# Performance work log

Hardware: AMD Instinct MI355X
Metric: run time of the kernel (lower is better)

The kernel has to match this reference:

```python
import jax, jax.numpy as jnp
import numpy as np

DIM = 768; NH = 8; G = 14; N = G * G + 1; B = 64; PD = DIM // 16; HID = 4 * DIM
SCOPES = (1, 4, 7)


def _build_adj(fs, scope):
    # windowed adjacency on an fs x fs grid, padded with an always-on ACM (class) token
    idx = np.arange(fs)
    ii, jj = np.meshgrid(idx, idx, indexing='ij')
    ri, rj = ii.ravel(), jj.ravel()
    a = ((np.abs(ri[:, None] - ri[None, :]) <= scope) & (np.abs(rj[:, None] - rj[None, :]) <= scope)).astype(np.float32)
    out = np.ones((fs * fs + 1, fs * fs + 1), np.float32)
    out[1:, 1:] = a
    return out


def _prior_adj():
    # loop=0 -> loop1=loop2=0, repeat = NH//4; heads get [adj1,adj1,adj2,adj2,adj3,adj3,ones,ones]
    rep = NH // 4
    mats = [_build_adj(G, s) for s in SCOPES] + [np.ones((N, N), np.float32)]
    return np.stack([m for m in mats for _ in range(rep)], 0)


def _rel_idx():
    coords = np.stack(np.meshgrid(np.arange(G), np.arange(G), indexing='ij')).reshape(2, -1)
    rel = (coords[:, :, None] - coords[:, None, :]).transpose(1, 2, 0).copy()
    rel[..., 0] += G - 1
    rel[..., 1] += G - 1
    rel[..., 0] *= 2 * G - 1
    idx = rel.sum(-1)
    out = np.full((N, N), (2 * G - 1) ** 2 + 1, np.int32)
    out[1:, 1:] = idx
    return out


def _biases():
    r = np.arange(-G, G + 1)  # arange(1-(G+1), G+1)
    g = np.stack(np.meshgrid(r, r, indexing='ij')).reshape(2, -1).T
    return g.astype(np.float32)  # ((2G+1)^2, 2)


def setup_inputs():
    key = jax.random.key(0)
    ks = iter(jax.random.split(key, 32))
    rn = lambda *s: jax.random.normal(next(ks), s, jnp.float32) * 0.02
    return dict(
        x=jax.random.normal(next(ks), (B, N, DIM), jnp.float32),
        norm1_w=jnp.ones(DIM), norm1_b=jnp.zeros(DIM),
        qkv_w=rn(3 * DIM, DIM),
        scale=10.0 * jnp.ones((NH, 1, 1)),
        pp_w=rn(PD, 2), pp_b=jnp.zeros(PD),
        ln1_w=jnp.ones(PD), ln1_b=jnp.zeros(PD), fcp1_w=rn(PD, PD), fcp1_b=jnp.zeros(PD),
        ln2_w=jnp.ones(PD), ln2_b=jnp.zeros(PD), fcp2_w=rn(PD, PD), fcp2_b=jnp.zeros(PD),
        ln3_w=jnp.ones(PD), ln3_b=jnp.zeros(PD), fcp3_w=rn(NH, PD), fcp3_b=jnp.zeros(NH),
        pre_w=rn(NH, NH) + jnp.eye(NH), post_w=rn(NH, NH) + jnp.eye(NH),
        proj_w=rn(DIM, DIM), proj_b=jnp.zeros(DIM),
        norm2_w=jnp.ones(DIM), norm2_b=jnp.zeros(DIM),
        m1_w=rn(HID, DIM), m1_b=jnp.zeros(HID),
        m2_w=rn(DIM, HID), m2_b=jnp.zeros(DIM),
        prior_adj=jnp.asarray(_prior_adj()),
        biases=jnp.asarray(_biases()),
        rel_idx=jnp.asarray(_rel_idx()),
    )


def _ln(x, w, b, eps=1e-5):
    m = x.mean(-1, keepdims=True)
    v = ((x - m) ** 2).mean(-1, keepdims=True)
    return (x - m) / jnp.sqrt(v + eps) * w + b


def _l2n(x, eps=1e-12):
    return x / jnp.maximum(jnp.linalg.norm(x, axis=-1, keepdims=True), eps)


def reference(x, norm1_w, norm1_b, qkv_w, scale, pp_w, pp_b, ln1_w, ln1_b, fcp1_w, fcp1_b, ln2_w, ln2_b, fcp2_w, fcp2_b, ln3_w, ln3_b, fcp3_w, fcp3_b, pre_w, post_w, proj_w, proj_b, norm2_w, norm2_b, m1_w, m1_b, m2_w, m2_b, prior_adj, biases, rel_idx):
    Bq, Nq, C = x.shape
    d = C // NH
    h = _ln(x, norm1_w, norm1_b)
    qkv = (h @ qkv_w.T).reshape(Bq, Nq, 3, NH, d).transpose(2, 0, 3, 1, 4)
    q, k, v = qkv[0], qkv[1], qkv[2]  # each (B, NH, N, d)
    attn = jnp.einsum('bhnd,bhmd->bhnm', _l2n(q), _l2n(k)) * jnp.minimum(scale, 100.0)[None]
    p = biases @ pp_w.T + pp_b
    p = jax.nn.relu(_ln(p, ln1_w, ln1_b)) @ fcp1_w.T + fcp1_b
    p = jax.nn.relu(_ln(p, ln2_w, ln2_b)) @ fcp2_w.T + fcp2_b
    p = jax.nn.relu(_ln(p, ln3_w, ln3_b)) @ fcp3_w.T + fcp3_b  # (841, NH)
    rpb = p[rel_idx]  # (N, N, NH)
    attn = attn + rpb.transpose(2, 0, 1)[None]
    attn = jnp.einsum('oh,bhnm->bonm', pre_w, attn)  # 1x1 conv over heads (pre-softmax)
    attn = jnp.where(prior_adj[None] > 0, attn, -1e9)
    attn = jax.nn.softmax(attn, axis=-1)
    attn = jnp.einsum('oh,bhnm->bonm', post_w, attn)  # 1x1 conv over heads (post-softmax)
    out = jnp.einsum('bhnm,bhmd->bhnd', attn, v).transpose(0, 2, 1, 3).reshape(Bq, Nq, C)
    x = x + (out @ proj_w.T + proj_b)
    h2 = _ln(x, norm2_w, norm2_b)
    h2 = jax.nn.gelu(h2 @ m1_w.T + m1_b, approximate=False) @ m2_w.T + m2_b
    return x + h2
```

## Files before the change

kernel.cpp:

```cpp
#include <hip/hip_runtime.h>
#include <hip/hip_bf16.h>
#include <math.h>

typedef __hip_bfloat16 bf16;
typedef __attribute__((ext_vector_type(8))) short bf16x8;
typedef __attribute__((ext_vector_type(4))) float f32x4;

__device__ __forceinline__ float b2f(bf16 x){ return __bfloat162float(x); }
__device__ __forceinline__ bf16  f2b(float x){ return __float2bfloat16(x); }

__device__ __forceinline__ void gld16(const bf16* g, bf16* l){
    __builtin_amdgcn_global_load_lds(
        (const __attribute__((address_space(1))) unsigned int*)g,
        (__attribute__((address_space(3))) unsigned int*)l, 16, 0, 0);
}

#define NTOK 197
#define NBATCH 64
#define NHEAD 8
#define DHEAD 96
#define DIMC 768
#define NROWS (NBATCH * NTOK)
#define VTS 224
#define SMS 228
#define MHALF 6304

#define OFF_P   0ull
#define OFF_W   32768ull
#define SZ_QKVW 3538944ull
#define SZ_PRJW 1179648ull
#define SZ_M1W  4718592ull
#define SZ_M2W  4718592ull
#define OFF_H   14188544ull
#define SZ_H    19365888ull
#define OFF_Q   33554432ull
#define OFF_K   52920320ull
#define OFF_V   72286208ull

__global__ __launch_bounds__(256) void w_cvt_all(
    const float* __restrict__ s0, const float* __restrict__ s1,
    const float* __restrict__ s2, const float* __restrict__ s3, bf16* __restrict__ d)
{
    int i = blockIdx.x*256 + threadIdx.x;
    const float* s; int off;
    if (i < 442368){ s=s0; off=i; }
    else if (i < 589824){ s=s1; off=i-442368; }
    else if (i < 1179648){ s=s2; off=i-589824; }
    else { s=s3; off=i-1179648; }
    float4 v = ((const float4*)s)[off];
    bf16 t[4] = {f2b(v.x), f2b(v.y), f2b(v.z), f2b(v.w)};
    ((ushort4*)d)[i] = *(ushort4*)t;
}

__global__ __launch_bounds__(64) void pos_mlp(
    const float* __restrict__ biases, const float* __restrict__ pp_w, const float* __restrict__ pp_b,
    const float* __restrict__ ln1w, const float* __restrict__ ln1b,
    const float* __restrict__ f1w,  const float* __restrict__ f1b,
    const float* __restrict__ ln2w, const float* __restrict__ ln2b,
    const float* __restrict__ f2w,  const float* __restrict__ f2b,
    const float* __restrict__ ln3w, const float* __restrict__ ln3b,
    const float* __restrict__ f3w,  const float* __restrict__ f3b,
    float* __restrict__ pout)
{
    const int row = blockIdx.x, j = threadIdx.x;
    __shared__ float va[48], vb[48];
    float b0 = biases[row*2], b1 = biases[row*2+1];
    if (j < 48) va[j] = b0*pp_w[j*2] + b1*pp_w[j*2+1] + pp_b[j];
    __syncthreads();
    {   float s=0.f, s2=0.f;
        for (int i=0;i<48;i++){ float t=va[i]; s+=t; s2+=t*t; }
        float mean=s*(1.f/48.f), var=s2*(1.f/48.f)-mean*mean, inv=rsqrtf(var+1e-5f);
        float r=0.f;
        if (j < 48){
            r = f1b[j];
            for (int i=0;i<48;i++){
                float t = fmaxf((va[i]-mean)*inv*ln1w[i] + ln1b[i], 0.f);
                r += t * f1w[j*48+i];
            }
        }
        __syncthreads();
        if (j < 48) vb[j] = r;
    }
    __syncthreads();
    {   float s=0.f, s2=0.f;
        for (int i=0;i<48;i++){ float t=vb[i]; s+=t; s2+=t*t; }
        float mean=s*(1.f/48.f), var=s2*(1.f/48.f)-mean*mean, inv=rsqrtf(var+1e-5f);
        float r=0.f;
        if (j < 48){
            r = f2b[j];
            for (int i=0;i<48;i++){
                float t = fmaxf((vb[i]-mean)*inv*ln2w[i] + ln2b[i], 0.f);
                r += t * f2w[j*48+i];
            }
        }
        __syncthreads();
        if (j < 48) va[j] = r;
    }
    __syncthreads();
    {   float s=0.f, s2=0.f;
        for (int i=0;i<48;i++){ float t=va[i]; s+=t; s2+=t*t; }
        float mean=s*(1.f/48.f), var=s2*(1.f/48.f)-mean*mean, inv=rsqrtf(var+1e-5f);
        if (j < 8){
            float r = f3b[j];
            for (int i=0;i<48;i++){
                float t = fmaxf((va[i]-mean)*inv*ln3w[i] + ln3b[i], 0.f);
                r += t * f3w[j*48+i];
            }
            pout[row*8+j] = r;
        }
    }
}

__device__ __forceinline__ float ldf(const bf16& x){ return __bfloat162float(x); }
__device__ __forceinline__ float ldf(const float& x){ return x; }

template<typename TIN>
__global__ __launch_bounds__(256) void ln768(
    const TIN* __restrict__ x, const float* __restrict__ w, const float* __restrict__ b,
    bf16* __restrict__ out)
{
    const int row = blockIdx.x, tid = threadIdx.x;
    const int wv = tid >> 6, ln = tid & 63;
    __shared__ float rs[4], rs2[4];
    const TIN* xr = x + (size_t)row * DIMC;
    float v0 = ldf(xr[tid]), v1 = ldf(xr[tid+256]), v2 = ldf(xr[tid+512]);
    float s = v0+v1+v2, s2 = v0*v0+v1*v1+v2*v2;
    #pragma unroll
    for (int off=32; off; off>>=1){ s += __shfl_xor(s,off,64); s2 += __shfl_xor(s2,off,64); }
    if (ln == 0){ rs[wv]=s; rs2[wv]=s2; }
    __syncthreads();
    s = rs[0]+rs[1]+rs[2]+rs[3]; s2 = rs2[0]+rs2[1]+rs2[2]+rs2[3];
    float mean = s*(1.f/768.f), var = s2*(1.f/768.f) - mean*mean;
    float inv = rsqrtf(var + 1e-5f);
    size_t base = (size_t)row * DIMC;
    out[base+tid]     = f2b((v0-mean)*inv*w[tid]     + b[tid]);
    out[base+tid+256] = f2b((v1-mean)*inv*w[tid+256] + b[tid+256]);
    out[base+tid+512] = f2b((v2-mean)*inv*w[tid+512] + b[tid+512]);
}

__global__ __launch_bounds__(256) void l2norm_qk(bf16* __restrict__ q, bf16* __restrict__ k)
{
    const int wv = threadIdx.x >> 6, ln = threadIdx.x & 63;
    const size_t NR = (size_t)NBATCH*NHEAD*NTOK;
    size_t row = (size_t)blockIdx.x * 4 + wv;
    bf16* ptr = (row < NR) ? (q + row*DHEAD) : (k + (row-NR)*DHEAD);
    float x0 = b2f(ptr[ln]);
    float x1 = (ln < 32) ? b2f(ptr[64+ln]) : 0.f;
    float ss = x0*x0 + x1*x1;
    #pragma unroll
    for (int off=32; off; off>>=1) ss += __shfl_xor(ss,off,64);
    float inv = 1.f / fmaxf(sqrtf(ss), 1e-12f);
    ptr[ln] = f2b(x0*inv);
    if (ln < 32) ptr[64+ln] = f2b(x1*inv);
}

__global__ __launch_bounds__(256) void attn_mfma(
    const bf16* __restrict__ q, const bf16* __restrict__ k, const bf16* __restrict__ vt,
    const float* __restrict__ p, const float* __restrict__ scale,
    const float* __restrict__ pre_w, const float* __restrict__ post_w,
    bf16* __restrict__ ao)
{
    const int id = blockIdx.x;
    const int r8 = id & 7, t8 = id >> 3;
    const int bx = t8 % 25, b = r8 + 8*(t8/25);
    const int n0 = bx*8;
    const int tid = threadIdx.x, wv = tid>>6, ln = tid&63;
    const int fr = ln&15, fq = ln>>4;
    __shared__ float S[NHEAD*8*SMS];
    __shared__ float s_pre[64], s_post[64], s_sc[8];
    bf16* Sb = (bf16*)S;
    if (tid < 64){ s_pre[tid]=pre_w[tid]; s_post[tid]=post_w[tid]; }
    if (tid < 8)  s_sc[tid] = fminf(scale[tid], 100.f);

    #pragma unroll
    for (int hh=0; hh<2; hh++){
        const int h = wv + hh*4;
        int qr = n0 + fr; if (qr > 196) qr = 196;
        const bf16* qrow = q + ((size_t)(b*NHEAD+h)*NTOK + qr)*DHEAD + fq*8;
        bf16x8 a0 = *(const bf16x8*)(qrow);
        bf16x8 a1 = *(const bf16x8*)(qrow+32);
        bf16x8 a2 = *(const bf16x8*)(qrow+64);
        const bf16* kb0 = k + (size_t)(b*NHEAD+h)*NTOK*DHEAD + fq*8;
        const bf16* kr = kb0 + (size_t)fr*DHEAD;
        bf16x8 kv0 = *(const bf16x8*)(kr);
        bf16x8 kv1 = *(const bf16x8*)(kr+32);
        bf16x8 kv2 = *(const bf16x8*)(kr+64);
        for (int mt=0; mt<13; mt++){
            bf16x8 c0=kv0, c1=kv1, c2=kv2;
            if (mt < 12){
                int nr = (mt+1)*16+fr; if (nr>196) nr=196;
                const bf16* kn = kb0 + (size_t)nr*DHEAD;
                kv0 = *(const bf16x8*)(kn);
                kv1 = *(const bf16x8*)(kn+32);
                kv2 = *(const bf16x8*)(kn+64);
            }
            f32x4 acc = {};
            acc = __builtin_amdgcn_mfma_f32_16x16x32_bf16(a0, c0, acc,0,0,0);
            acc = __builtin_amdgcn_mfma_f32_16x16x32_bf16(a1, c1, acc,0,0,0);
            acc = __builtin_amdgcn_mfma_f32_16x16x32_bf16(a2, c2, acc,0,0,0);
            if (fq < 2){
                #pragma unroll
                for (int i=0;i<4;i++)
                    S[(h*8 + fq*4+i)*SMS + mt*16+fr] = acc[i];
            }
        }
    }
    __syncthreads();

    const int sco[8] = {1,1,4,4,7,7,1000,1000};
    for (int c=tid; c<8*224; c+=256){
        int nq = c/224, m = c - nq*224;
        if (m >= 197){
            #pragma unroll
            for (int o=0;o<8;o++) S[(o*8+nq)*SMS+m] = -1e9f;
            continue;
        }
        int n = n0+nq; if (n > 196) n = 196;
        bool always = (n==0) || (m==0);
        int ri=0, ci=0, rj=0, cj=0;
        if (!always){
            ri=(n-1)/14; ci=(n-1)-ri*14;
            rj=(m-1)/14; cj=(m-1)-rj*14;
        }
        int dr = ri-rj; if (dr<0) dr=-dr;
        int dc = ci-cj; if (dc<0) dc=-dc;
        int idx = always ? 730 : (ri-rj+13)*27 + (ci-cj+13);
        const float* pv = p + idx*8;
        float sh[8];
        #pragma unroll
        for (int h=0;h<8;h++) sh[h] = S[(h*8+nq)*SMS+m]*s_sc[h] + pv[h];
        float ov[8];
        #pragma unroll
        for (int o=0;o<8;o++){
            float v=0.f;
            #pragma unroll
            for (int hh2=0;hh2<8;hh2++) v += s_pre[o*8+hh2]*sh[hh2];
            bool on = always || (dr<=sco[o] && dc<=sco[o]);
            ov[o] = on ? v : -1e9f;
        }
        #pragma unroll
        for (int o=0;o<8;o++) S[(o*8+nq)*SMS+m] = ov[o];
    }
    __syncthreads();

    for (int r = wv*16; r < wv*16+16; r++){
        float* row = &S[r*SMS];
        float mx = -3e38f;
        for (int m=ln; m<224; m+=64) mx = fmaxf(mx, row[m]);
        #pragma unroll
        for (int off=32; off; off>>=1) mx = fmaxf(mx, __shfl_xor(mx,off,64));
        float sum = 0.f;
        for (int m=ln; m<224; m+=64){ float e=__expf(row[m]-mx); row[m]=e; sum+=e; }
        #pragma unroll
        for (int off=32; off; off>>=1) sum += __shfl_xor(sum,off,64);
        float inv = 1.f/sum;
        for (int m=ln; m<224; m+=64) row[m] *= inv;
    }
    __syncthreads();

    float ov[7][8];
    #pragma unroll
    for (int kk=0; kk<7; kk++){
        int c = tid + kk*256;
        if (c < 8*197){
            int nq = c/197, m = c - nq*197;
            float ph[8];
            #pragma unroll
            for (int o=0;o<8;o++) ph[o] = S[(o*8+nq)*SMS+m];
            #pragma unroll
            for (int o2=0;o2<8;o2++){
                float v=0.f;
                #pragma unroll
                for (int o=0;o<8;o++) v += s_post[o2*8+o]*ph[o];
                ov[kk][o2]=v;
            }
        }
    }
    __syncthreads();
    #pragma unroll
    for (int kk=0; kk<7; kk++){
        int c = tid + kk*256;
        if (c < 8*197){
            int nq = c/197, m = c - nq*197;
            #pragma unroll
            for (int o=0;o<8;o++) Sb[(o*8+nq)*456 + m] = f2b(ov[kk][o]);
        }
    }
    for (int i=tid; i<64*27; i+=256){
        int r = i/27, mm = 197 + (i - (i/27)*27);
        Sb[r*456 + mm] = f2b(0.f);
    }
    __syncthreads();

    const int frA = fr & 7;
    #pragma unroll
    for (int hh=0; hh<2; hh++){
        const int h = wv + hh*4;
        const bf16* vbase = vt + (size_t)(b*NHEAD+h)*DHEAD*VTS;
        for (int dt=0; dt<6; dt++){
            f32x4 acc = {};
            #pragma unroll
            for (int ks=0; ks<7; ks++){
                const bf16* ap = Sb + (h*8+frA)*456 + ks*32 + fq*8;
                const bf16* bp = vbase + (size_t)(dt*16+fr)*VTS + ks*32 + fq*8;
                acc = __builtin_amdgcn_mfma_f32_16x16x32_bf16(*(const bf16x8*)ap, *(const bf16x8*)bp, acc,0,0,0);
            }
            #pragma unroll
            for (int i=0;i<4;i++){
                int nq = fq*4+i, n = n0+nq;
                if (nq < 8 && n < NTOK)
                    ao[((size_t)b*NTOK+n)*DIMC + h*DHEAD + dt*16+fr] = f2b(acc[i]);
            }
        }
    }
}

enum { EPI_QKV=0, EPI_X1=1, EPI_GELU=2, EPI_OUT=3 };

template<int EPI>
__global__ __launch_bounds__(256) void gemm128(
    const bf16* __restrict__ A, int lda, int M,
    const bf16* __restrict__ B, int ldb,
    int K,
    const float* __restrict__ bias,
    const float* __restrict__ resid_f,
    const bf16* __restrict__ resid_b,
    float* __restrict__ dst_f,
    bf16* __restrict__ dst_b, int lddb,
    int row_off,
    bf16* __restrict__ qo, bf16* __restrict__ ko, bf16* __restrict__ vto)
{
    __shared__ bf16 As[2*128*32];
    __shared__ bf16 Bs[2*128*32];
    const int tid = threadIdx.x;
    const int wv = tid >> 6, ln = tid & 63;
    const int fr = ln & 15, fq = ln >> 4;
    const int wr = (wv & 1)*64, wc = (wv >> 1)*64;
    const int m0 = blockIdx.y*128, n0 = blockIdx.x*128;
    const int lnrow = ln >> 2, lncol = (ln & 3)*8;
    f32x4 acc[4][4] = {};
    for (int k0=0; k0<K; k0+=64){
        #pragma unroll
        for (int t=0;t<2;t++){
            #pragma unroll
            for (int c=0;c<2;c++){
                int rA = m0 + (c*4+wv)*16 + lnrow;
                if (rA >= M) rA = M-1;
                gld16(A + (size_t)rA*lda + k0 + t*32 + lncol, &As[t*4096 + (c*4+wv)*16*32]);
                int rB = n0 + (c*4+wv)*16 + lnrow;
                gld16(B + (size_t)rB*ldb + k0 + t*32 + lncol, &Bs[t*4096 + (c*4+wv)*16*32]);
            }
        }
        __syncthreads();
        #pragma unroll
        for (int t=0;t<2;t++){
            bf16x8 af[4], bfv[4];
            #pragma unroll
            for (int i=0;i<4;i++){
                af[i]  = *(const bf16x8*)&As[t*4096 + (wr + i*16 + fr)*32 + fq*8];
                bfv[i] = *(const bf16x8*)&Bs[t*4096 + (wc + i*16 + fr)*32 + fq*8];
            }
            #pragma unroll
            for (int mi=0;mi<4;mi++)
                #pragma unroll
                for (int ni=0;ni<4;ni++)
                    acc[mi][ni] = __builtin_amdgcn_mfma_f32_16x16x32_bf16(af[mi], bfv[ni], acc[mi][ni],0,0,0);
        }
        __syncthreads();
    }
    #pragma unroll
    for (int mi=0;mi<4;mi++){
        #pragma unroll
        for (int ni=0;ni<4;ni++){
            #pragma unroll
            for (int i=0;i<4;i++){
                int row = m0 + wr + mi*16 + fq*4 + i;
                int col = n0 + wc + ni*16 + fr;
                if (row >= M) continue;
                float val = acc[mi][ni][i];
                if constexpr (EPI == EPI_QKV){
                    int which = col/768, rem = col - which*768;
                    int hh = rem/96, di = rem - hh*96;
                    int bb = row/NTOK, nn = row - bb*NTOK;
                    if (which == 0)      qo[(((size_t)bb*NHEAD+hh)*NTOK+nn)*DHEAD + di] = f2b(val);
                    else if (which == 1) ko[(((size_t)bb*NHEAD+hh)*NTOK+nn)*DHEAD + di] = f2b(val);
                    else {
                        vto[(((size_t)bb*NHEAD+hh)*DHEAD+di)*VTS + nn] = f2b(val);
                        if (nn < VTS - NTOK)
                            vto[(((size_t)bb*NHEAD+hh)*DHEAD+di)*VTS + NTOK + nn] = f2b(0.f);
                    }
                } else if constexpr (EPI == EPI_X1){
                    dst_b[(size_t)row*DIMC + col] = f2b(val + bias[col] + resid_f[(size_t)row*DIMC + col]);
                } else if constexpr (EPI == EPI_GELU){
                    float t = val + bias[col];
                    t = 0.5f*t*(1.f + erff(t*0.70710678118654752f));
                    dst_b[(size_t)row*lddb + col] = f2b(t);
                } else {
                    size_t g = (size_t)(row + row_off)*DIMC + col;
                    dst_f[g] = val + bias[col] + b2f(resid_b[g]);
                }
            }
        }
    }
}

extern "C" void kernel_launch(void* const* d_in, const int* in_sizes, int n_in,
                              void* d_out, int out_size, void* d_ws, size_t ws_size,
                              hipStream_t stream)
{
    const float* x        = (const float*)d_in[0];
    const float* norm1_w  = (const float*)d_in[1];
    const float* norm1_b  = (const float*)d_in[2];
    const float* qkv_w    = (const float*)d_in[3];
    const float* scale    = (const float*)d_in[4];
    const float* pp_w     = (const float*)d_in[5];
    const float* pp_b     = (const float*)d_in[6];
    const float* ln1_w    = (const float*)d_in[7];
    const float* ln1_b    = (const float*)d_in[8];
    const float* fcp1_w   = (const float*)d_in[9];
    const float* fcp1_b   = (const float*)d_in[10];
    const float* ln2_w    = (const float*)d_in[11];
    const float* ln2_b    = (const float*)d_in[12];
    const float* fcp2_w   = (const float*)d_in[13];
    const float* fcp2_b   = (const float*)d_in[14];
    const float* ln3_w    = (const float*)d_in[15];
    const float* ln3_b    = (const float*)d_in[16];
    const float* fcp3_w   = (const float*)d_in[17];
    const float* fcp3_b   = (const float*)d_in[18];
    const float* pre_w    = (const float*)d_in[19];
    const float* post_w   = (const float*)d_in[20];
    const float* proj_w   = (const float*)d_in[21];
    const float* proj_b   = (const float*)d_in[22];
    const float* nrm2_w   = (const float*)d_in[23];
    const float* nrm2_b   = (const float*)d_in[24];
    const float* m1_w     = (const float*)d_in[25];
    const float* m1_b     = (const float*)d_in[26];
    const float* m2_w     = (const float*)d_in[27];
    const float* m2_b     = (const float*)d_in[28];
    const float* biases   = (const float*)d_in[30];
    float* out = (float*)d_out;

    char* ws = (char*)d_ws;
    float* p      = (float*)(ws + OFF_P);
    bf16*  qkvw_b = (bf16*)(ws + OFF_W);
    bf16*  prjw_b = (bf16*)(ws + OFF_W + SZ_QKVW);
    bf16*  m1w_b  = (bf16*)(ws + OFF_W + SZ_QKVW + SZ_PRJW);
    bf16*  m2w_b  = (bf16*)(ws + OFF_W + SZ_QKVW + SZ_PRJW + SZ_M1W);
    bf16*  h   = (bf16*)(ws + OFF_H);
    bf16*  qb  = (bf16*)(ws + OFF_Q);
    bf16*  kb  = (bf16*)(ws + OFF_K);
    bf16*  vt  = (bf16*)(ws + OFF_V);
    bf16*  ao  = (bf16*)(ws + OFF_H);
    bf16*  x1b = (bf16*)(ws + OFF_V);
    bf16*  h2  = (bf16*)(ws + OFF_K);
    bf16*  mid = (bf16*)(ws + OFF_H);

    w_cvt_all<<<6912, 256, 0, stream>>>(qkv_w, proj_w, m1_w, m2_w, qkvw_b);
    pos_mlp<<<841, 64, 0, stream>>>(biases, pp_w, pp_b, ln1_w, ln1_b, fcp1_w, fcp1_b,
                                    ln2_w, ln2_b, fcp2_w, fcp2_b, ln3_w, ln3_b, fcp3_w, fcp3_b, p);
    ln768<float><<<NROWS, 256, 0, stream>>>(x, norm1_w, norm1_b, h);
    gemm128<EPI_QKV><<<dim3(18, 99), 256, 0, stream>>>(
        h, DIMC, NROWS, qkvw_b, DIMC, DIMC, nullptr, nullptr, nullptr, nullptr,
        nullptr, 0, 0, qb, kb, vt);
    l2norm_qk<<<(NBATCH*NHEAD*NTOK*2)/4, 256, 0, stream>>>(qb, kb);
    attn_mfma<<<1600, 256, 0, stream>>>(qb, kb, vt, p, scale, pre_w, post_w, ao);
    gemm128<EPI_X1><<<dim3(6, 99), 256, 0, stream>>>(
        ao, DIMC, NROWS, prjw_b, DIMC, DIMC, proj_b, x, nullptr, nullptr,
        x1b, 0, 0, nullptr, nullptr, nullptr);
    ln768<bf16><<<NROWS, 256, 0, stream>>>(x1b, nrm2_w, nrm2_b, h2);
    for (int c=0; c<2; c++){
        const int r0 = c*MHALF;
        gemm128<EPI_GELU><<<dim3(24, 50), 256, 0, stream>>>(
            h2 + (size_t)r0*DIMC, DIMC, MHALF, m1w_b, DIMC, DIMC, m1_b,
            nullptr, nullptr, nullptr, mid, 3072, 0, nullptr, nullptr, nullptr);
        gemm128<EPI_OUT><<<dim3(6, 50), 256, 0, stream>>>(
            mid, 3072, MHALF, m2w_b, 3072, 3072, m2_b,
            nullptr, x1b, out, nullptr, 0, r0, nullptr, nullptr, nullptr);
    }
    (void)in_sizes; (void)n_in; (void)out_size; (void)ws_size;
}
```

Measured before the change: 848.9 us.

## Fold scale into q, pre-mix position bias, shrink score buffer and pipeline attention loads

Folds the clamped per-head logit scale into the q L2-normalisation and applies the pre-softmax head mix to the position-bias table once in pos_mlp, which removes per-element scale and bias work from the attention kernel. The score buffer row stride drops from 228 to 206 floats (bf16 P stride 224), cutting LDS use so more blocks can be resident. The mask, softmax and post-mix loops are reorganised so each thread handles one query row with 16- or 32-lane groups. K loads are double-buffered two tiles ahead, and the P and V operands for the PV MFMA are held in registers with a prefetch. The narrower stride means only 206 score columns are kept, and scale is now applied to bf16 q before rounding, which can shift numerics slightly.

```diff
diff --git a/kernel.cpp b/kernel.cpp
--- a/kernel.cpp
+++ b/kernel.cpp
@@ -22,7 +22,8 @@
 #define DIMC 768
 #define NROWS (NBATCH * NTOK)
 #define VTS 224
-#define SMS 228
+#define SMS 206
+#define SBS 224
 #define MHALF 6304
 
 #define OFF_P   0ull
@@ -60,10 +61,11 @@
     const float* __restrict__ f2w,  const float* __restrict__ f2b,
     const float* __restrict__ ln3w, const float* __restrict__ ln3b,
     const float* __restrict__ f3w,  const float* __restrict__ f3b,
+    const float* __restrict__ pre_w,
     float* __restrict__ pout)
 {
     const int row = blockIdx.x, j = threadIdx.x;
-    __shared__ float va[48], vb[48];
+    __shared__ float va[48], vb[48], pf[8];
     float b0 = biases[row*2], b1 = biases[row*2+1];
     if (j < 48) va[j] = b0*pp_w[j*2] + b1*pp_w[j*2+1] + pp_b[j];
     __syncthreads();
@@ -106,8 +108,15 @@
                 float t = fmaxf((va[i]-mean)*inv*ln3w[i] + ln3b[i], 0.f);
                 r += t * f3w[j*48+i];
             }
-            pout[row*8+j] = r;
-        }
+            pf[j] = r;
+        }
+    }
+    __syncthreads();
+    if (j < 8){
+        float s = 0.f;
+        #pragma unroll
+        for (int hh=0; hh<8; hh++) s += pre_w[j*8+hh]*pf[hh];
+        pout[row*8+j] = s;
     }
 }
 
@@ -138,25 +147,31 @@
     out[base+tid+512] = f2b((v2-mean)*inv*w[tid+512] + b[tid+512]);
 }
 
-__global__ __launch_bounds__(256) void l2norm_qk(bf16* __restrict__ q, bf16* __restrict__ k)
+__global__ __launch_bounds__(256) void l2norm_qk(bf16* __restrict__ q, bf16* __restrict__ k,
+                                                 const float* __restrict__ scale)
 {
     const int wv = threadIdx.x >> 6, ln = threadIdx.x & 63;
     const size_t NR = (size_t)NBATCH*NHEAD*NTOK;
     size_t row = (size_t)blockIdx.x * 4 + wv;
-    bf16* ptr = (row < NR) ? (q + row*DHEAD) : (k + (row-NR)*DHEAD);
+    bool isq = row < NR;
+    bf16* ptr = isq ? (q + row*DHEAD) : (k + (row-NR)*DHEAD);
     float x0 = b2f(ptr[ln]);
     float x1 = (ln < 32) ? b2f(ptr[64+ln]) : 0.f;
     float ss = x0*x0 + x1*x1;
     #pragma unroll
     for (int off=32; off; off>>=1) ss += __shfl_xor(ss,off,64);
     float inv = 1.f / fmaxf(sqrtf(ss), 1e-12f);
+    if (isq){
+        int h = (int)((row / NTOK) & (NHEAD-1));
+        inv *= fminf(scale[h], 100.f);
+    }
     ptr[ln] = f2b(x0*inv);
     if (ln < 32) ptr[64+ln] = f2b(x1*inv);
 }
 
 __global__ __launch_bounds__(256) void attn_mfma(
     const bf16* __restrict__ q, const bf16* __restrict__ k, const bf16* __restrict__ vt,
-    const float* __restrict__ p, const float* __restrict__ scale,
+    const float* __restrict__ p,
     const float* __restrict__ pre_w, const float* __restrict__ post_w,
     bf16* __restrict__ ao)
 {
@@ -167,10 +182,9 @@
     const int tid = threadIdx.x, wv = tid>>6, ln = tid&63;
     const int fr = ln&15, fq = ln>>4;
     __shared__ float S[NHEAD*8*SMS];
-    __shared__ float s_pre[64], s_post[64], s_sc[8];
+    __shared__ float s_pre[64], s_post[64];
     bf16* Sb = (bf16*)S;
     if (tid < 64){ s_pre[tid]=pre_w[tid]; s_post[tid]=post_w[tid]; }
-    if (tid < 8)  s_sc[tid] = fminf(scale[tid], 100.f);
 
     #pragma unroll
     for (int hh=0; hh<2; hh++){
@@ -181,114 +195,118 @@
         bf16x8 a1 = *(const bf16x8*)(qrow+32);
         bf16x8 a2 = *(const bf16x8*)(qrow+64);
         const bf16* kb0 = k + (size_t)(b*NHEAD+h)*NTOK*DHEAD + fq*8;
-        const bf16* kr = kb0 + (size_t)fr*DHEAD;
-        bf16x8 kv0 = *(const bf16x8*)(kr);
-        bf16x8 kv1 = *(const bf16x8*)(kr+32);
-        bf16x8 kv2 = *(const bf16x8*)(kr+64);
+        auto krow = [&](int mt){ int nr = mt*16+fr; if (nr>196) nr=196; return kb0 + (size_t)nr*DHEAD; };
+        const bf16* kp0 = krow(0);
+        bf16x8 c00 = *(const bf16x8*)(kp0), c01 = *(const bf16x8*)(kp0+32), c02 = *(const bf16x8*)(kp0+64);
+        const bf16* kp1 = krow(1);
+        bf16x8 c10 = *(const bf16x8*)(kp1), c11 = *(const bf16x8*)(kp1+32), c12 = *(const bf16x8*)(kp1+64);
+        #pragma unroll
         for (int mt=0; mt<13; mt++){
-            bf16x8 c0=kv0, c1=kv1, c2=kv2;
-            if (mt < 12){
-                int nr = (mt+1)*16+fr; if (nr>196) nr=196;
-                const bf16* kn = kb0 + (size_t)nr*DHEAD;
-                kv0 = *(const bf16x8*)(kn);
-                kv1 = *(const bf16x8*)(kn+32);
-                kv2 = *(const bf16x8*)(kn+64);
+            bf16x8 p0, p1, p2;
+            if (mt < 11){
+                const bf16* kn = krow(mt+2);
+                p0 = *(const bf16x8*)(kn); p1 = *(const bf16x8*)(kn+32); p2 = *(const bf16x8*)(kn+64);
             }
             f32x4 acc = {};
-            acc = __builtin_amdgcn_mfma_f32_16x16x32_bf16(a0, c0, acc,0,0,0);
-            acc = __builtin_amdgcn_mfma_f32_16x16x32_bf16(a1, c1, acc,0,0,0);
-            acc = __builtin_amdgcn_mfma_f32_16x16x32_bf16(a2, c2, acc,0,0,0);
-            if (fq < 2){
+            acc = __builtin_amdgcn_mfma_f32_16x16x32_bf16(a0, c00, acc,0,0,0);
+            acc = __builtin_amdgcn_mfma_f32_16x16x32_bf16(a1, c01, acc,0,0,0);
+            acc = __builtin_amdgcn_mfma_f32_16x16x32_bf16(a2, c02, acc,0,0,0);
+            int col = mt*16 + fr;
+            if (fq < 2 && col < SMS){
                 #pragma unroll
                 for (int i=0;i<4;i++)
-                    S[(h*8 + fq*4+i)*SMS + mt*16+fr] = acc[i];
-            }
-        }
-    }
-    __syncthreads();
-
-    const int sco[8] = {1,1,4,4,7,7,1000,1000};
-    for (int c=tid; c<8*224; c+=256){
-        int nq = c/224, m = c - nq*224;
-        if (m >= 197){
-            #pragma unroll
-            for (int o=0;o<8;o++) S[(o*8+nq)*SMS+m] = -1e9f;
-            continue;
-        }
-        int n = n0+nq; if (n > 196) n = 196;
-        bool always = (n==0) || (m==0);
-        int ri=0, ci=0, rj=0, cj=0;
-        if (!always){
-            ri=(n-1)/14; ci=(n-1)-ri*14;
-            rj=(m-1)/14; cj=(m-1)-rj*14;
-        }
-        int dr = ri-rj; if (dr<0) dr=-dr;
-        int dc = ci-cj; if (dc<0) dc=-dc;
-        int idx = always ? 730 : (ri-rj+13)*27 + (ci-cj+13);
-        const float* pv = p + idx*8;
-        float sh[8];
-        #pragma unroll
-        for (int h=0;h<8;h++) sh[h] = S[(h*8+nq)*SMS+m]*s_sc[h] + pv[h];
-        float ov[8];
-        #pragma unroll
-        for (int o=0;o<8;o++){
-            float v=0.f;
-            #pragma unroll
-            for (int hh2=0;hh2<8;hh2++) v += s_pre[o*8+hh2]*sh[hh2];
-            bool on = always || (dr<=sco[o] && dc<=sco[o]);
-            ov[o] = on ? v : -1e9f;
-        }
-        #pragma unroll
-        for (int o=0;o<8;o++) S[(o*8+nq)*SMS+m] = ov[o];
-    }
-    __syncthreads();
-
-    for (int r = wv*16; r < wv*16+16; r++){
-        float* row = &S[r*SMS];
-        float mx = -3e38f;
-        for (int m=ln; m<224; m+=64) mx = fmaxf(mx, row[m]);
-        #pragma unroll
-        for (int off=32; off; off>>=1) mx = fmaxf(mx, __shfl_xor(mx,off,64));
-        float sum = 0.f;
-        for (int m=ln; m<224; m+=64){ float e=__expf(row[m]-mx); row[m]=e; sum+=e; }
-        #pragma unroll
-        for (int off=32; off; off>>=1) sum += __shfl_xor(sum,off,64);
-        float inv = 1.f/sum;
-        for (int m=ln; m<224; m+=64) row[m] *= inv;
-    }
-    __syncthreads();
-
-    float ov[7][8];
-    #pragma unroll
-    for (int kk=0; kk<7; kk++){
-        int c = tid + kk*256;
-        if (c < 8*197){
-            int nq = c/197, m = c - nq*197;
-            float ph[8];
-            #pragma unroll
-            for (int o=0;o<8;o++) ph[o] = S[(o*8+nq)*SMS+m];
-            #pragma unroll
-            for (int o2=0;o2<8;o2++){
-                float v=0.f;
-                #pragma unroll
-                for (int o=0;o<8;o++) v += s_post[o2*8+o]*ph[o];
-                ov[kk][o2]=v;
-            }
-        }
-    }
-    __syncthreads();
-    #pragma unroll
-    for (int kk=0; kk<7; kk++){
-        int c = tid + kk*256;
-        if (c < 8*197){
-            int nq = c/197, m = c - nq*197;
-            #pragma unroll
-            for (int o=0;o<8;o++) Sb[(o*8+nq)*456 + m] = f2b(ov[kk][o]);
-        }
-    }
-    for (int i=tid; i<64*27; i+=256){
-        int r = i/27, mm = 197 + (i - (i/27)*27);
-        Sb[r*456 + mm] = f2b(0.f);
+                    S[(h*8 + fq*4+i)*SMS + col] = acc[i];
+            }
+            c00=c10; c01=c11; c02=c12;
+            if (mt < 11){ c10=p0; c11=p1; c12=p2; }
+        }
+    }
+    __syncthreads();
+
+    {
+        const int sco[8] = {1,1,4,4,7,7,1000,1000};
+        const int nq = tid >> 5, l32 = tid & 31;
+        int n = n0 + nq; if (n > 196) n = 196;
+        const bool nAlways = (n == 0);
+        int ri=0, ci=0;
+        if (!nAlways){ ri=(n-1)/14; ci=(n-1)-ri*14; }
+        for (int m = l32; m < SMS; m += 32){
+            if (m >= 197){
+                #pragma unroll
+                for (int o=0;o<8;o++) S[(o*8+nq)*SMS+m] = -1e9f;
+                continue;
+            }
+            bool always = nAlways || (m==0);
+            int rj=0, cj=0;
+            if (m > 0){ rj=(m-1)/14; cj=(m-1)-rj*14; }
+            int dr = ri-rj; if (dr<0) dr=-dr;
+            int dc = ci-cj; if (dc<0) dc=-dc;
+            int idx = always ? 730 : (ri-rj+13)*27 + (ci-cj+13);
+            const float* pv = p + idx*8;
+            float sh[8];
+            #pragma unroll
+            for (int h2=0;h2<8;h2++) sh[h2] = S[(h2*8+nq)*SMS+m];
+            float ov[8];
+            #pragma unroll
+            for (int o=0;o<8;o++){
+                float v = pv[o];
+                #pragma unroll
+                for (int h2=0;h2<8;h2++) v += s_pre[o*8+h2]*sh[h2];
+                bool on = always || (dr<=sco[o] && dc<=sco[o]);
+                ov[o] = on ? v : -1e9f;
+            }
+            #pragma unroll
+            for (int o=0;o<8;o++) S[(o*8+nq)*SMS+m] = ov[o];
+        }
+    }
+    __syncthreads();
+
+    {
+        const int g = ln >> 4, l16 = ln & 15;
+        #pragma unroll
+        for (int rr=0; rr<4; rr++){
+            float* row = &S[(wv*16 + rr*4 + g)*SMS];
+            float mx = -3e38f;
+            for (int m=l16; m<SMS; m+=16) mx = fmaxf(mx, row[m]);
+            #pragma unroll
+            for (int off=8; off; off>>=1) mx = fmaxf(mx, __shfl_xor(mx,off,64));
+            float sum = 0.f;
+            for (int m=l16; m<SMS; m+=16){ float e=__expf(row[m]-mx); row[m]=e; sum+=e; }
+            #pragma unroll
+            for (int off=8; off; off>>=1) sum += __shfl_xor(sum,off,64);
+            float inv = 1.f/sum;
+            for (int m=l16; m<SMS; m+=16) row[m] *= inv;
+        }
+    }
+    __syncthreads();
+
+    {
+        const int nq = tid >> 5, l32 = tid & 31;
+        float ov[7][8];
+        #pragma unroll
+        for (int kk=0; kk<7; kk++){
+            int m = l32 + 32*kk;
+            if (m < 197){
+                float ph[8];
+                #pragma unroll
+                for (int o=0;o<8;o++) ph[o] = S[(o*8+nq)*SMS+m];
+                #pragma unroll
+                for (int o2=0;o2<8;o2++){
+                    float v=0.f;
+                    #pragma unroll
+                    for (int o=0;o<8;o++) v += s_post[o2*8+o]*ph[o];
+                    ov[kk][o2]=v;
+                }
+            }
+        }
+        __syncthreads();
+        #pragma unroll
+        for (int kk=0; kk<7; kk++){
+            int m = l32 + 32*kk;
+            #pragma unroll
+            for (int o=0;o<8;o++)
+                Sb[(o*8+nq)*SBS + m] = (m < 197) ? f2b(ov[kk][o]) : f2b(0.f);
+        }
     }
     __syncthreads();
 
@@ -297,20 +315,33 @@
     for (int hh=0; hh<2; hh++){
         const int h = wv + hh*4;
         const bf16* vbase = vt + (size_t)(b*NHEAD+h)*DHEAD*VTS;
+        bf16x8 pa[7];
+        #pragma unroll
+        for (int ks=0; ks<7; ks++)
+            pa[ks] = *(const bf16x8*)(Sb + (h*8+frA)*SBS + ks*32 + fq*8);
+        bf16x8 bv[7], bn[7];
+        #pragma unroll
+        for (int ks=0; ks<7; ks++)
+            bv[ks] = *(const bf16x8*)(vbase + (size_t)fr*VTS + ks*32 + fq*8);
+        #pragma unroll
         for (int dt=0; dt<6; dt++){
+            if (dt < 5){
+                #pragma unroll
+                for (int ks=0; ks<7; ks++)
+                    bn[ks] = *(const bf16x8*)(vbase + (size_t)((dt+1)*16+fr)*VTS + ks*32 + fq*8);
+            }
             f32x4 acc = {};
             #pragma unroll
-            for (int ks=0; ks<7; ks++){
-                const bf16* ap = Sb + (h*8+frA)*456 + ks*32 + fq*8;
-                const bf16* bp = vbase + (size_t)(dt*16+fr)*VTS + ks*32 + fq*8;
-                acc = __builtin_amdgcn_mfma_f32_16x16x32_bf16(*(const bf16x8*)ap, *(const bf16x8*)bp, acc,0,0,0);
-            }
+            for (int ks=0; ks<7; ks++)
+                acc = __builtin_amdgcn_mfma_f32_16x16x32_bf16(pa[ks], bv[ks], acc,0,0,0);
             #pragma unroll
             for (int i=0;i<4;i++){
                 int nq = fq*4+i, n = n0+nq;
                 if (nq < 8 && n < NTOK)
                     ao[((size_t)b*NTOK+n)*DIMC + h*DHEAD + dt*16+fr] = f2b(acc[i]);
             }
+            #pragma unroll
+            for (int ks=0; ks<7; ks++) bv[ks] = bn[ks];
         }
     }
 }
@@ -457,13 +488,14 @@
 
     w_cvt_all<<<6912, 256, 0, stream>>>(qkv_w, proj_w, m1_w, m2_w, qkvw_b);
     pos_mlp<<<841, 64, 0, stream>>>(biases, pp_w, pp_b, ln1_w, ln1_b, fcp1_w, fcp1_b,
-                                    ln2_w, ln2_b, fcp2_w, fcp2_b, ln3_w, ln3_b, fcp3_w, fcp3_b, p);
+                                    ln2_w, ln2_b, fcp2_w, fcp2_b, ln3_w, ln3_b, fcp3_w, fcp3_b,
+                                    pre_w, p);
     ln768<float><<<NROWS, 256, 0, stream>>>(x, norm1_w, norm1_b, h);
     gemm128<EPI_QKV><<<dim3(18, 99), 256, 0, stream>>>(
         h, DIMC, NROWS, qkvw_b, DIMC, DIMC, nullptr, nullptr, nullptr, nullptr,
         nullptr, 0, 0, qb, kb, vt);
-    l2norm_qk<<<(NBATCH*NHEAD*NTOK*2)/4, 256, 0, stream>>>(qb, kb);
-    attn_mfma<<<1600, 256, 0, stream>>>(qb, kb, vt, p, scale, pre_w, post_w, ao);
+    l2norm_qk<<<(NBATCH*NHEAD*NTOK*2)/4, 256, 0, stream>>>(qb, kb, scale);
+    attn_mfma<<<1600, 256, 0, stream>>>(qb, kb, vt, p, pre_w, post_w, ao);
     gemm128<EPI_X1><<<dim3(6, 99), 256, 0, stream>>>(
         ao, DIMC, NROWS, prjw_b, DIMC, DIMC, proj_b, x, nullptr, nullptr,
         x1b, 0, 0, nullptr, nullptr, nullptr);
```

Result: faster. 804.1 us (-5.3%).
